# Optimization experiments

Measured on AMD Instinct MI355X. Metric: run time of the kernel, lower is better.

Reference implementation:

```python
import jax, jax.numpy as jnp
import numpy as np

NFFT = 512
HOP = 256
N_FREQ = NFFT // 2


def _imdct_kernels():
    # Matches _get_imdct_kernels: windowed IMDCT cosine basis, shape [nfft, nfft//2]
    def kernel_fn(time, freq):
        win = np.sin(np.pi * (2 * time + 1) / (2.0 * NFFT))
        return np.cos(np.pi / NFFT * (2 * time + 1 + NFFT / 2.0) * (freq + 0.5)) * win
    k = np.fromfunction(kernel_fn, (NFFT, N_FREQ), dtype=np.float64)
    return jnp.asarray(k.astype(np.float32))  # [nfft, n_freq]


def setup_inputs() -> dict:
    key = jax.random.key(0)
    spec = jax.random.normal(key, (16, 1, N_FREQ, 4096), dtype=jnp.float32)
    return {"spec": spec, "kernels": _imdct_kernels()}


def reference(spec, kernels):
    # spec: [B, 1, n_freq, T]; kernels: [nfft, n_freq]
    B, _, _, T = spec.shape
    # conv2d with (n_freq,1) kernel == per-frame basis matmul over frequency
    frames = jnp.einsum('bft,kf->btk', spec[:, 0], kernels) * (4.0 / NFFT)  # [B, T, nfft]
    # conv_transpose2d with identity-diagonal kernel and stride=hop == overlap-add
    L = (T - 1) * HOP + NFFT
    idx = jnp.arange(T)[:, None] * HOP + jnp.arange(NFFT)[None, :]  # [T, nfft]
    out = jnp.zeros((B, L), dtype=spec.dtype).at[:, idx].add(frames)
    return out
```

## Files before the change

kernel.cpp:

```cpp
#include <hip/hip_runtime.h>
#include <stdint.h>

#define NFREQ 256
#define NB 16
#define NT 4096
#define LOUT 1048832
#define TROWS 65
#define TROW 132

typedef __bf16 bf16;
typedef __bf16 bf16x8 __attribute__((ext_vector_type(8)));
typedef float floatx4 __attribute__((ext_vector_type(4)));

__device__ inline uint32_t f_as_u(float x) { union { float f; uint32_t u; } v; v.f = x; return v.u; }
__device__ inline uint32_t bf16r(float x) {
    uint32_t u = f_as_u(x);
    return (u + 0x7fffu + ((u >> 16) & 1u)) >> 16;
}

__global__ __launch_bounds__(256) void build_kb(const float* __restrict__ ker,
                                                bf16* __restrict__ kbF) {
    int idx = blockIdx.x * 256 + threadIdx.x;
    int n = idx >> 9, f = idx & 511;
    float v = (f < 256) ? ker[(n + 256) * 256 + f] : ker[n * 256 + (f - 256)];
    uint32_t rr = bf16r(v * 0.0078125f);
    union { uint16_t u; bf16 b; } o; o.u = (uint16_t)rr;
    kbF[((size_t)(f >> 5) * 256 + n) * 32 + (f & 31)] = o.b;
}

__global__ __launch_bounds__(256, 4) void imdct_gemm(const float* __restrict__ spec,
                                                     const bf16* __restrict__ kbF,
                                                     float* __restrict__ out) {
    __shared__ uint32_t Tt[TROWS * TROW];

    const int jt = blockIdx.x;
    const int b  = blockIdx.y;
    const int tid = threadIdx.x, lane = tid & 63, w = tid >> 6;
    const int j0 = jt * 64;
    const float* sb = spec + (size_t)b * NFREQ * NT;

    {
        const int lpar = lane & 1, lt = lane >> 1;
        const int fpw = w * 32;
        for (int rb = 0; rb < 4; ++rb) {
            float v[16];
            #pragma unroll
            for (int i = 0; i < 16; ++i) {
                int r = rb * 16 + i;
                int tc = r >> 5, fpi = r & 31;
                int f = (fpw + fpi) * 2 + lpar;
                int t = j0 - 1 + tc * 32 + lt;
                v[i] = ((unsigned)t < (unsigned)NT) ? sb[(size_t)f * NT + t] : 0.0f;
            }
            #pragma unroll
            for (int i = 0; i < 16; i += 2) {
                int r = rb * 16 + i;
                int tc = r >> 5, fpi = r & 31;
                int tl = tc * 32 + lt;
                uint32_t h0 = bf16r(v[i]);     uint32_t o0 = (uint32_t)__shfl_xor((int)h0, 1);
                uint32_t h1 = bf16r(v[i + 1]); uint32_t o1 = (uint32_t)__shfl_xor((int)h1, 1);
                if (lpar == 0) {
                    uint2 pk; pk.x = (h0 & 0xffffu) | (o0 << 16); pk.y = (h1 & 0xffffu) | (o1 << 16);
                    *reinterpret_cast<uint2*>(&Tt[tl * TROW + fpw + fpi]) = pk;
                }
            }
        }
        int f = w * 64 + lane;
        int t = j0 + 63;
        float v = ((unsigned)t < (unsigned)NT) ? sb[(size_t)f * NT + t] : 0.0f;
        uint32_t h = bf16r(v); uint32_t o = (uint32_t)__shfl_xor((int)h, 1);
        if (lpar == 0) Tt[64 * TROW + w * 32 + lt] = (h & 0xffffu) | (o << 16);
    }
    __syncthreads();

    const int row16 = lane & 15, q = lane >> 4;
    floatx4 acc[4][4] = {};
    const uint8_t* Tb = reinterpret_cast<const uint8_t*>(Tt);
    const bf16* kbw = kbF + (size_t)w * 64 * 32;

    for (int kki = 0; kki < 8; ++kki) {
        const int toff = (kki >= 4) ? 1 : 0;
        const int kbyte = (kki & 3) * 128;
        #pragma unroll
        for (int ks = 0; ks < 2; ++ks) {
            const int kchunk = kki * 2 + ks;
            bf16x8 af[4], bfr[4];
            #pragma unroll
            for (int i = 0; i < 4; ++i)
                af[i] = *reinterpret_cast<const bf16x8*>(
                    Tb + (size_t)(i * 16 + row16 + toff) * 528 + kbyte + ks * 64 + q * 16);
            #pragma unroll
            for (int jn = 0; jn < 4; ++jn)
                bfr[jn] = *reinterpret_cast<const bf16x8*>(
                    kbw + (size_t)kchunk * 8192 + (jn * 16 + row16) * 32 + q * 8);
            #pragma unroll
            for (int i = 0; i < 4; ++i)
                #pragma unroll
                for (int jn = 0; jn < 4; ++jn)
                    acc[i][jn] = __builtin_amdgcn_mfma_f32_16x16x32_bf16(af[i], bfr[jn], acc[i][jn], 0, 0, 0);
        }
    }

    #pragma unroll
    for (int i = 0; i < 4; ++i) {
        #pragma unroll
        for (int e = 0; e < 4; ++e) {
            int j = j0 + i * 16 + q * 4 + e;
            if (j <= 4096) {
                float* orow = out + (size_t)b * LOUT + (size_t)j * 256 + w * 64;
                #pragma unroll
                for (int jn = 0; jn < 4; ++jn)
                    orow[jn * 16 + row16] = acc[i][jn][e];
            }
        }
    }
}

extern "C" void kernel_launch(void* const* d_in, const int* in_sizes, int n_in,
                              void* d_out, int out_size, void* d_ws, size_t ws_size,
                              hipStream_t stream) {
    const float* spec = (const float*)d_in[0];
    const float* ker  = (const float*)d_in[1];
    float* out = (float*)d_out;

    bf16* kbF = (bf16*)d_ws;

    build_kb<<<512, 256, 0, stream>>>(ker, kbF);
    imdct_gemm<<<dim3(65, NB), 256, 0, stream>>>(spec, kbF, out);
}
```

Before: 142.7 us.

## Process two time tiles per block, staging the second tile during the first GEMM

```diff
diff --git a/kernel.cpp b/kernel.cpp
--- a/kernel.cpp
+++ b/kernel.cpp
@@ -28,91 +28,131 @@
     kbF[((size_t)(f >> 5) * 256 + n) * 32 + (f & 31)] = o.b;
 }
 
-__global__ __launch_bounds__(256, 4) void imdct_gemm(const float* __restrict__ spec,
+#define STAGE_GROUP(TtB, J0, rb) { \
+    float v_[16]; \
+    _Pragma("unroll") \
+    for (int i_ = 0; i_ < 16; ++i_) { \
+        int r_ = (rb) * 16 + i_; int tc_ = r_ >> 5, fpi_ = r_ & 31; \
+        int f_ = (fpw + fpi_) * 2 + lpar; \
+        int t_ = (J0) - 1 + tc_ * 32 + lt; \
+        v_[i_] = ((unsigned)t_ < (unsigned)NT) ? sb[(size_t)f_ * NT + t_] : 0.0f; } \
+    _Pragma("unroll") \
+    for (int i_ = 0; i_ < 16; i_ += 2) { \
+        int r_ = (rb) * 16 + i_; int tc_ = r_ >> 5, fpi_ = r_ & 31; \
+        int tl_ = tc_ * 32 + lt; \
+        uint32_t h0_ = bf16r(v_[i_]);     uint32_t o0_ = (uint32_t)__shfl_xor((int)h0_, 1); \
+        uint32_t h1_ = bf16r(v_[i_ + 1]); uint32_t o1_ = (uint32_t)__shfl_xor((int)h1_, 1); \
+        if (lpar == 0) { \
+            uint2 pk_; pk_.x = (h0_ & 0xffffu) | (o0_ << 16); pk_.y = (h1_ & 0xffffu) | (o1_ << 16); \
+            *reinterpret_cast<uint2*>(&(TtB)[tl_ * TROW + fpw + fpi_]) = pk_; } } }
+
+#define STAGE_ROW64(TtB, J0) { \
+    int f_ = w * 64 + lane; int te_ = (J0) + 63; \
+    float v_ = ((unsigned)te_ < (unsigned)NT) ? sb[(size_t)f_ * NT + te_] : 0.0f; \
+    uint32_t h_ = bf16r(v_); uint32_t o_ = (uint32_t)__shfl_xor((int)h_, 1); \
+    if (lpar == 0) (TtB)[64 * TROW + w * 32 + lt] = (h_ & 0xffffu) | (o_ << 16); }
+
+#define LOADB(dst, kc) { \
+    _Pragma("unroll") \
+    for (int jn_ = 0; jn_ < 4; ++jn_) \
+        dst[jn_] = *reinterpret_cast<const bf16x8*>( \
+            kbw + (size_t)(kc) * 8192 + (jn_ * 16 + row16) * 32 + q * 8); }
+
+#define LOADA(dst, Tb, kki, ks) { \
+    _Pragma("unroll") \
+    for (int i_ = 0; i_ < 4; ++i_) \
+        dst[i_] = *reinterpret_cast<const bf16x8*>( \
+            (Tb) + (size_t)(i_ * 16 + row16 + ((kki) >= 4 ? 1 : 0)) * 528 \
+                 + ((kki) & 3) * 128 + (ks) * 64 + q * 16); }
+
+#define DOMFMA(af_, bf_) { \
+    _Pragma("unroll") \
+    for (int i_ = 0; i_ < 4; ++i_) \
+        _Pragma("unroll") \
+        for (int jn_ = 0; jn_ < 4; ++jn_) \
+            acc[i_][jn_] = __builtin_amdgcn_mfma_f32_16x16x32_bf16(af_[i_], bf_[jn_], acc[i_][jn_], 0, 0, 0); }
+
+#define STORE_TILE(J0) { \
+    _Pragma("unroll") \
+    for (int i_ = 0; i_ < 4; ++i_) { \
+        _Pragma("unroll") \
+        for (int e_ = 0; e_ < 4; ++e_) { \
+            int j_ = (J0) + i_ * 16 + q * 4 + e_; \
+            if (j_ <= 4096) { \
+                float* orow_ = out + (size_t)b * LOUT + (size_t)j_ * 256 + w * 64; \
+                _Pragma("unroll") \
+                for (int jn_ = 0; jn_ < 4; ++jn_) \
+                    orow_[jn_ * 16 + row16] = acc[i_][jn_][e_]; } } } }
+
+__global__ __launch_bounds__(256, 2) void imdct_gemm(const float* __restrict__ spec,
                                                      const bf16* __restrict__ kbF,
                                                      float* __restrict__ out) {
-    __shared__ uint32_t Tt[TROWS * TROW];
+    __shared__ uint32_t Tt[2][TROWS * TROW];
 
-    const int jt = blockIdx.x;
     const int b  = blockIdx.y;
     const int tid = threadIdx.x, lane = tid & 63, w = tid >> 6;
-    const int j0 = jt * 64;
+    const int j0t0 = blockIdx.x * 128;
+    const int j0t1 = j0t0 + 64;
+    const bool has1 = (blockIdx.x < 32);
     const float* sb = spec + (size_t)b * NFREQ * NT;
 
+    const int lpar = lane & 1, lt = lane >> 1;
+    const int fpw = w * 32;
+    const int row16 = lane & 15, q = lane >> 4;
+    const bf16* kbw = kbF + (size_t)w * 64 * 32;
+    uint32_t* Tt0 = &Tt[0][0];
+    uint32_t* Tt1 = &Tt[1][0];
+
+    STAGE_GROUP(Tt0, j0t0, 0);
+    STAGE_GROUP(Tt0, j0t0, 1);
+    STAGE_GROUP(Tt0, j0t0, 2);
+    STAGE_GROUP(Tt0, j0t0, 3);
+    STAGE_ROW64(Tt0, j0t0);
+    __syncthreads();
+
+    floatx4 acc[4][4] = {};
     {
-        const int lpar = lane & 1, lt = lane >> 1;
-        const int fpw = w * 32;
-        for (int rb = 0; rb < 4; ++rb) {
-            float v[16];
-            #pragma unroll
-            for (int i = 0; i < 16; ++i) {
-                int r = rb * 16 + i;
-                int tc = r >> 5, fpi = r & 31;
-                int f = (fpw + fpi) * 2 + lpar;
-                int t = j0 - 1 + tc * 32 + lt;
-                v[i] = ((unsigned)t < (unsigned)NT) ? sb[(size_t)f * NT + t] : 0.0f;
+        const uint8_t* Tb = reinterpret_cast<const uint8_t*>(Tt0);
+        #pragma unroll
+        for (int kki = 0; kki < 8; ++kki) {
+            if (has1) {
+                if (kki == 0) STAGE_GROUP(Tt1, j0t1, 0);
+                if (kki == 1) STAGE_GROUP(Tt1, j0t1, 1);
+                if (kki == 2) STAGE_GROUP(Tt1, j0t1, 2);
+                if (kki == 3) STAGE_GROUP(Tt1, j0t1, 3);
+                if (kki == 4) STAGE_ROW64(Tt1, j0t1);
             }
-            #pragma unroll
-            for (int i = 0; i < 16; i += 2) {
-                int r = rb * 16 + i;
-                int tc = r >> 5, fpi = r & 31;
-                int tl = tc * 32 + lt;
-                uint32_t h0 = bf16r(v[i]);     uint32_t o0 = (uint32_t)__shfl_xor((int)h0, 1);
-                uint32_t h1 = bf16r(v[i + 1]); uint32_t o1 = (uint32_t)__shfl_xor((int)h1, 1);
-                if (lpar == 0) {
-                    uint2 pk; pk.x = (h0 & 0xffffu) | (o0 << 16); pk.y = (h1 & 0xffffu) | (o1 << 16);
-                    *reinterpret_cast<uint2*>(&Tt[tl * TROW + fpw + fpi]) = pk;
-                }
-            }
+            bf16x8 af[4], bfr[4];
+            LOADB(bfr, kki * 2 + 0);
+            LOADA(af, Tb, kki, 0);
+            DOMFMA(af, bfr);
+            LOADB(bfr, kki * 2 + 1);
+            LOADA(af, Tb, kki, 1);
+            DOMFMA(af, bfr);
         }
-        int f = w * 64 + lane;
-        int t = j0 + 63;
-        float v = ((unsigned)t < (unsigned)NT) ? sb[(size_t)f * NT + t] : 0.0f;
-        uint32_t h = bf16r(v); uint32_t o = (uint32_t)__shfl_xor((int)h, 1);
-        if (lpar == 0) Tt[64 * TROW + w * 32 + lt] = (h & 0xffffu) | (o << 16);
     }
     __syncthreads();
 
-    const int row16 = lane & 15, q = lane >> 4;
-    floatx4 acc[4][4] = {};
-    const uint8_t* Tb = reinterpret_cast<const uint8_t*>(Tt);
-    const bf16* kbw = kbF + (size_t)w * 64 * 32;
+    STORE_TILE(j0t0);
 
-    for (int kki = 0; kki < 8; ++kki) {
-        const int toff = (kki >= 4) ? 1 : 0;
-        const int kbyte = (kki & 3) * 128;
+    if (has1) {
         #pragma unroll
-        for (int ks = 0; ks < 2; ++ks) {
-            const int kchunk = kki * 2 + ks;
-            bf16x8 af[4], bfr[4];
-            #pragma unroll
-            for (int i = 0; i < 4; ++i)
-                af[i] = *reinterpret_cast<const bf16x8*>(
-                    Tb + (size_t)(i * 16 + row16 + toff) * 528 + kbyte + ks * 64 + q * 16);
+        for (int i = 0; i < 4; ++i)
             #pragma unroll
             for (int jn = 0; jn < 4; ++jn)
-                bfr[jn] = *reinterpret_cast<const bf16x8*>(
-                    kbw + (size_t)kchunk * 8192 + (jn * 16 + row16) * 32 + q * 8);
-            #pragma unroll
-            for (int i = 0; i < 4; ++i)
-                #pragma unroll
-                for (int jn = 0; jn < 4; ++jn)
-                    acc[i][jn] = __builtin_amdgcn_mfma_f32_16x16x32_bf16(af[i], bfr[jn], acc[i][jn], 0, 0, 0);
+                acc[i][jn] = (floatx4){0.f, 0.f, 0.f, 0.f};
+        const uint8_t* Tb = reinterpret_cast<const uint8_t*>(Tt1);
+        #pragma unroll
+        for (int kki = 0; kki < 8; ++kki) {
+            bf16x8 af[4], bfr[4];
+            LOADB(bfr, kki * 2 + 0);
+            LOADA(af, Tb, kki, 0);
+            DOMFMA(af, bfr);
+            LOADB(bfr, kki * 2 + 1);
+            LOADA(af, Tb, kki, 1);
+            DOMFMA(af, bfr);
         }
-    }
-
-    #pragma unroll
-    for (int i = 0; i < 4; ++i) {
-        #pragma unroll
-        for (int e = 0; e < 4; ++e) {
-            int j = j0 + i * 16 + q * 4 + e;
-            if (j <= 4096) {
-                float* orow = out + (size_t)b * LOUT + (size_t)j * 256 + w * 64;
-                #pragma unroll
-                for (int jn = 0; jn < 4; ++jn)
-                    orow[jn * 16 + row16] = acc[i][jn][e];
-            }
-        }
+        STORE_TILE(j0t1);
     }
 }
 
@@ -126,5 +166,5 @@
     bf16* kbF = (bf16*)d_ws;
 
     build_kb<<<512, 256, 0, stream>>>(ker, kbF);
-    imdct_gemm<<<dim3(65, NB), 256, 0, stream>>>(spec, kbF, out);
+    imdct_gemm<<<dim3(33, NB), 256, 0, stream>>>(spec, kbF, out);
 }
```

Result: no change. 145.5 us (+2.0%).
